# Optimization experiments

Hardware: AMD Instinct MI355X
Metric: run time of the kernel (lower is better)

Reference implementation:

```python
import jax, jax.numpy as jnp
import numpy as np
import math

EMBED_DIM = 1024
NUM_HEADS = 16
HEAD_DIM = EMBED_DIM // NUM_HEADS
B, S = 2, 2048


def setup_inputs() -> dict:
    key = jax.random.key(0)
    ks = jax.random.split(key, 13)
    sc = 1.0 / math.sqrt(EMBED_DIM)
    inp = {
        "query": jax.random.normal(ks[0], (B, S, EMBED_DIM), jnp.float32),
        "key": jax.random.normal(ks[1], (B, S, EMBED_DIM), jnp.float32),
        "value": jax.random.normal(ks[2], (B, S, EMBED_DIM), jnp.float32),
        "input_patch_mask": jax.random.randint(ks[3], (B, S), 0, 2, jnp.int32),
        "Wq": jax.random.normal(ks[4], (EMBED_DIM, EMBED_DIM), jnp.float32) * sc,
        "bq": jnp.zeros((EMBED_DIM,), jnp.float32),
        "Wk": jax.random.normal(ks[5], (EMBED_DIM, EMBED_DIM), jnp.float32) * sc,
        "bk": jnp.zeros((EMBED_DIM,), jnp.float32),
        "Wv": jax.random.normal(ks[6], (EMBED_DIM, EMBED_DIM), jnp.float32) * sc,
        "bv": jnp.zeros((EMBED_DIM,), jnp.float32),
        "Wo": jax.random.normal(ks[7], (EMBED_DIM, EMBED_DIM), jnp.float32) * sc,
        "bo": jnp.zeros((EMBED_DIM,), jnp.float32),
    }
    return inp


def _masked_softmax(scores, mask):
    # Equivalent to masked_fill(-inf) -> softmax -> nan_to_num(0.0):
    # fully-masked rows produce exactly 0, without generating NaNs.
    neg_inf = jnp.array(-jnp.inf, scores.dtype)
    s = jnp.where(mask, scores, neg_inf)
    m = jnp.max(s, axis=-1, keepdims=True)
    m_safe = jnp.where(jnp.isfinite(m), m, jnp.zeros_like(m))
    e = jnp.where(mask, jnp.exp(s - m_safe), 0.0)
    denom = jnp.sum(e, axis=-1, keepdims=True)
    denom = jnp.where(denom == 0.0, 1.0, denom)
    return e / denom


def reference(query, key, value, input_patch_mask, Wq, bq, Wk, bk, Wv, bv, Wo, bo):
    b, s, d = query.shape
    h, hd = NUM_HEADS, HEAD_DIM
    q = (query @ Wq.T + bq).reshape(b, s, h, hd).transpose(0, 2, 1, 3)  # [b,h,s,hd]
    k = (key @ Wk.T + bk).reshape(b, s, h, hd).transpose(0, 2, 1, 3)
    v = (value @ Wv.T + bv).reshape(b, s, h, hd).transpose(0, 2, 1, 3)
    scores = jnp.einsum("bhqd,bhkd->bhqk", q, k) / math.sqrt(hd)
    # mask[b,i,j] = patch_mask[b,i] * patch_mask[b,j]
    mask = (input_patch_mask[:, :, None] * input_patch_mask[:, None, :]) > 0
    attn = _masked_softmax(scores, mask[:, None, :, :])  # dropout in eval mode = identity
    context = jnp.einsum("bhqk,bhkd->bhqd", attn, v)
    context = context.transpose(0, 2, 1, 3).reshape(b, s, d)
    return context @ Wo.T + bo
```

## Files before the change

kernel.cpp:

```cpp
#include <hip/hip_runtime.h>
#include <cstdint>
#include <cstddef>

#define EMBED 1024
#define NHEAD 16
#define HD    64
#define BATCH 2
#define SEQ   2048
#define MROWS (BATCH*SEQ)
#define QSCALE 0.1803368801111137f

typedef __bf16 bf16;
typedef __bf16 bf16x8 __attribute__((ext_vector_type(8)));
typedef float  f32x4  __attribute__((ext_vector_type(4)));
typedef unsigned int u32;

#if __has_builtin(__builtin_amdgcn_exp2f)
#define EXP2(x) __builtin_amdgcn_exp2f(x)
#else
#define EXP2(x) exp2f(x)
#endif

typedef const u32 __attribute__((address_space(1)))* gp_t;
typedef u32 __attribute__((address_space(3)))* lp_t;

__device__ __forceinline__ void g2l16(const void* g, void* l) {
  __builtin_amdgcn_global_load_lds((gp_t)(uintptr_t)g, (lp_t)(u32)(uintptr_t)l, 16, 0, 0);
}

#define MFMA(a, b, c) __builtin_amdgcn_mfma_f32_16x16x32_bf16((a), (b), (c), 0, 0, 0)

#define SZX8 ((MROWS*EMBED)/8)
#define SZW8 ((EMBED*EMBED)/8)

__global__ void cast_all(const float* __restrict__ q, const float* __restrict__ k,
                         const float* __restrict__ v, const float* __restrict__ wq,
                         const float* __restrict__ wk, const float* __restrict__ wv,
                         const float* __restrict__ wo,
                         bf16* xq, bf16* xk, bf16* xv,
                         bf16* wqb, bf16* wkb, bf16* wvb, bf16* wob) {
  int z = blockIdx.y;
  const float* in; bf16* out;
  switch (z) {
    case 0: in = q;  out = xq;  break;
    case 1: in = k;  out = xk;  break;
    case 2: in = v;  out = xv;  break;
    case 3: in = wq; out = wqb; break;
    case 4: in = wk; out = wkb; break;
    case 5: in = wv; out = wvb; break;
    default: in = wo; out = wob; break;
  }
  int n8 = (z < 3) ? SZX8 : SZW8;
  int i = blockIdx.x * blockDim.x + threadIdx.x;
  if (i >= n8) return;
  const float4* p = (const float4*)in;
  float4 a = p[2*i], b = p[2*i+1];
  union { bf16 h[8]; uint4 u; } r;
  r.h[0] = (bf16)a.x; r.h[1] = (bf16)a.y; r.h[2] = (bf16)a.z; r.h[3] = (bf16)a.w;
  r.h[4] = (bf16)b.x; r.h[5] = (bf16)b.y; r.h[6] = (bf16)b.z; r.h[7] = (bf16)b.w;
  ((uint4*)out)[i] = r.u;
}

#define BM 128
#define BN 128
#define BK 32
#define NKI (EMBED/BK)

__device__ __forceinline__ void gemm_core(
    const bf16* __restrict__ A, const bf16* __restrict__ W,
    bf16* Al, bf16* Bl, f32x4 (&acc)[4][4])
{
  const int tid  = threadIdx.x;
  const int lane = tid & 63, wid = tid >> 6;
  const int quad = lane >> 4, l16 = lane & 15;
  const int wm = wid >> 1, wn = wid & 1;
  const int m0 = blockIdx.y * BM, n0 = blockIdx.x * BN;

  const int R = tid >> 2, Cc = tid & 3;
  const int gcol = (Cc ^ ((R >> 1) & 3)) * 8;
  const bf16* Ag = A + (size_t)(m0 + R) * EMBED + gcol;
  const bf16* Bg = W + (size_t)(n0 + R) * EMBED + gcol;
  bf16* AlW = Al + wid * 512;
  bf16* BlW = Bl + wid * 512;

  g2l16(Ag, AlW);                      g2l16(Ag + (size_t)64*EMBED, AlW + 2048);
  g2l16(Bg, BlW);                      g2l16(Bg + (size_t)64*EMBED, BlW + 2048);
  __syncthreads();

  for (int ki = 0; ki < NKI; ++ki) {
    const int cur = ki & 1;
    if (ki + 1 < NKI) {
      const int nb = cur ^ 1;
      const int k0 = (ki + 1) * BK;
      g2l16(Ag + k0, AlW + nb*4096);
      g2l16(Ag + (size_t)64*EMBED + k0, AlW + nb*4096 + 2048);
      g2l16(Bg + k0, BlW + nb*4096);
      g2l16(Bg + (size_t)64*EMBED + k0, BlW + nb*4096 + 2048);
    }
    const bf16* Ac = Al + cur*4096;
    const bf16* Bc = Bl + cur*4096;
    bf16x8 af[4], bg[4];
#pragma unroll
    for (int i = 0; i < 4; ++i) {
      int ra = wm*64 + i*16 + l16;
      af[i] = *(const bf16x8*)(Ac + ra*32 + ((quad ^ ((ra>>1)&3))*8));
      int rb = wn*64 + i*16 + l16;
      bg[i] = *(const bf16x8*)(Bc + rb*32 + ((quad ^ ((rb>>1)&3))*8));
    }
#pragma unroll
    for (int i = 0; i < 4; ++i)
#pragma unroll
      for (int j = 0; j < 4; ++j)
        acc[i][j] = MFMA(af[i], bg[j], acc[i][j]);
    __syncthreads();
  }
}

__global__ __launch_bounds__(256) void qkv_kernel(
    const bf16* __restrict__ Xq, const bf16* __restrict__ Xk, const bf16* __restrict__ Xv,
    const bf16* __restrict__ Wq, const bf16* __restrict__ Wk, const bf16* __restrict__ Wv,
    const float* __restrict__ bq, const float* __restrict__ bk, const float* __restrict__ bv,
    bf16* __restrict__ Qp, bf16* __restrict__ Kp, bf16* __restrict__ VTg)
{
  __shared__ bf16 Al[2*BM*BK];
  __shared__ bf16 Bl[2*BN*BK];
  const int z = blockIdx.z;
  const bf16* A = z==0 ? Xq : z==1 ? Xk : Xv;
  const bf16* W = z==0 ? Wq : z==1 ? Wk : Wv;
  const float* bias = z==0 ? bq : z==1 ? bk : bv;
  const float scale = (z==0) ? QSCALE : 1.0f;

  f32x4 acc[4][4] = {};
  gemm_core(A, W, Al, Bl, acc);

  const int lane = threadIdx.x & 63, wid = threadIdx.x >> 6;
  const int quad = lane >> 4, l16 = lane & 15;
  const int wm = wid >> 1, wn = wid & 1;
  const int m0 = blockIdx.y * BM, n0 = blockIdx.x * BN;

#pragma unroll
  for (int i = 0; i < 4; ++i) {
#pragma unroll
    for (int j = 0; j < 4; ++j) {
      int col = n0 + wn*64 + j*16 + l16;
      float bv2 = bias[col];
      if (z < 2) {
        bf16* outp = (z == 0) ? Qp : Kp;
#pragma unroll
        for (int r = 0; r < 4; ++r) {
          int row = m0 + wm*64 + i*16 + quad*4 + r;
          outp[(size_t)row*EMBED + col] = (bf16)((acc[i][j][r] + bv2) * scale);
        }
      } else {
        int row0 = m0 + wm*64 + i*16 + quad*4;
        int bb = row0 >> 11, ss0 = row0 & (SEQ-1);
        int hh = col >> 6, dd = col & (HD-1);
        const size_t base = (((size_t)bb*NHEAD + hh)*HD + dd)*SEQ;
#pragma unroll
        for (int r = 0; r < 4; ++r) {
          int s = ss0 + r;
          int tile = s >> 6, loc = s & 63;
          int p = ((loc & 15) << 2) | (loc >> 4);
          VTg[base + tile*64 + p] = (bf16)(acc[i][j][r] + bv2);
        }
      }
    }
  }
}

__global__ __launch_bounds__(256) void oproj_kernel(
    const bf16* __restrict__ Ctx, const bf16* __restrict__ Wo,
    const float* __restrict__ bo, float* __restrict__ out)
{
  __shared__ bf16 Al[2*128*32];
  __shared__ bf16 Bl[2*64*32];
  const int tid  = threadIdx.x;
  const int lane = tid & 63, wid = tid >> 6;
  const int quad = lane >> 4, l16 = lane & 15;
  const int m0 = blockIdx.y * 128, n0 = blockIdx.x * 64;

  const int R = tid >> 2, Cc = tid & 3;
  const int gcol = (Cc ^ ((R >> 1) & 3)) * 8;
  const bf16* Ag = Ctx + (size_t)(m0 + R) * EMBED + gcol;
  const bf16* Bg = Wo  + (size_t)(n0 + R) * EMBED + gcol;
  bf16* AlW = Al + wid * 512;
  bf16* BlW = Bl + wid * 512;

  g2l16(Ag, AlW);  g2l16(Ag + (size_t)64*EMBED, AlW + 2048);
  g2l16(Bg, BlW);
  __syncthreads();

  f32x4 acc[2][4] = {};
  for (int ki = 0; ki < NKI; ++ki) {
    const int cur = ki & 1;
    if (ki + 1 < NKI) {
      const int nb = cur ^ 1;
      const int k0 = (ki + 1) * BK;
      g2l16(Ag + k0, AlW + nb*4096);
      g2l16(Ag + (size_t)64*EMBED + k0, AlW + nb*4096 + 2048);
      g2l16(Bg + k0, BlW + nb*2048);
    }
    const bf16* Ac = Al + cur*4096;
    const bf16* Bc = Bl + cur*2048;
    bf16x8 af[2], bg[4];
#pragma unroll
    for (int u = 0; u < 2; ++u) {
      int ra = wid*32 + u*16 + l16;
      af[u] = *(const bf16x8*)(Ac + ra*32 + ((quad ^ ((ra>>1)&3))*8));
    }
#pragma unroll
    for (int j = 0; j < 4; ++j) {
      int rb = j*16 + l16;
      bg[j] = *(const bf16x8*)(Bc + rb*32 + ((quad ^ ((rb>>1)&3))*8));
    }
#pragma unroll
    for (int u = 0; u < 2; ++u)
#pragma unroll
      for (int j = 0; j < 4; ++j)
        acc[u][j] = MFMA(af[u], bg[j], acc[u][j]);
    __syncthreads();
  }

#pragma unroll
  for (int u = 0; u < 2; ++u)
#pragma unroll
    for (int j = 0; j < 4; ++j) {
      int col = n0 + j*16 + l16;
      float bv = bo[col];
#pragma unroll
      for (int r = 0; r < 4; ++r) {
        int row = m0 + wid*32 + u*16 + quad*4 + r;
        out[(size_t)row*EMBED + col] = (acc[u][j][r] + bv);
      }
    }
}

#define NT  (SEQ/64)
#define PST 72

__global__ __launch_bounds__(256, 3) void attn_kernel(
    const bf16* __restrict__ Qp, const bf16* __restrict__ Kp, const bf16* __restrict__ VT,
    const int* __restrict__ pmask, bf16* __restrict__ Ctx)
{
  __shared__ bf16 Kt[2][64*64];
  __shared__ bf16 Vt[2][64*64];
  __shared__ bf16 Pl[4][32*PST];

  const int qt = blockIdx.x, h = blockIdx.y, b = blockIdx.z;
  const int tid = threadIdx.x, lane = tid & 63, wid = tid >> 6;
  const int quad = lane >> 4, l16 = lane & 15;
  const int qrow0 = qt*128 + wid*32;

  bf16x8 qf[2][2];
#pragma unroll
  for (int u = 0; u < 2; ++u) {
    const size_t qoff = (size_t)(b*SEQ + qrow0 + u*16 + l16)*EMBED + h*HD;
    qf[u][0] = *(const bf16x8*)(Qp + qoff + quad*8);
    qf[u][1] = *(const bf16x8*)(Qp + qoff + 32 + quad*8);
  }

  int qm[2][4];
#pragma unroll
  for (int u = 0; u < 2; ++u)
#pragma unroll
    for (int r = 0; r < 4; ++r) qm[u][r] = pmask[b*SEQ + qrow0 + u*16 + quad*4 + r];

  bf16 onev = (bf16)1.0f;
  bf16x8 ones = {onev, onev, onev, onev, onev, onev, onev, onev};

  const bf16* Kg  = Kp + (size_t)b*SEQ*EMBED + h*HD;
  const bf16* VTg = VT + (size_t)(b*NHEAD + h)*HD*SEQ;

  const int R = tid >> 3;
  const int Cc = tid & 7;
  const int scol = (Cc ^ (R & 7)) * 8;

  f32x4 o[2][4] = {};
  f32x4 lacc[2] = {};

#define STAGE(kt, buf) do {                                              \
    const bf16* kg = Kg + (size_t)((kt)*64 + R)*EMBED + scol;            \
    const bf16* vg = VTg + (size_t)R*SEQ + (kt)*64 + scol;               \
    bf16* kl = &Kt[buf][0] + wid*512;                                    \
    bf16* vl = &Vt[buf][0] + wid*512;                                    \
    g2l16(kg, kl);  g2l16(kg + (size_t)32*EMBED, kl + 2048);             \
    g2l16(vg, vl);  g2l16(vg + (size_t)32*SEQ,   vl + 2048);             \
  } while (0)

  STAGE(0, 0);
  __syncthreads();

  for (int kt = 0; kt < NT; ++kt) {
    const int cur = kt & 1;
    if (kt + 1 < NT) STAGE(kt + 1, cur ^ 1);
    const bf16* Kc = &Kt[cur][0];
    const bf16* Vc = &Vt[cur][0];

    f32x4 sg[2][4];
#pragma unroll
    for (int g = 0; g < 4; ++g) {
      int ra = g*16 + l16, sa = ra & 7;
      bf16x8 kfa = *(const bf16x8*)(Kc + ra*64 + ((quad     ^ sa)*8));
      bf16x8 kfb = *(const bf16x8*)(Kc + ra*64 + (((quad+4) ^ sa)*8));
      int km = pmask[b*SEQ + kt*64 + g*16 + l16];
#pragma unroll
      for (int u = 0; u < 2; ++u) {
        f32x4 s = {};
        s = MFMA(qf[u][0], kfa, s);
        s = MFMA(qf[u][1], kfb, s);
#pragma unroll
        for (int r = 0; r < 4; ++r) sg[u][g][r] = km ? EXP2(s[r]) : 0.0f;
      }
    }

#pragma unroll
    for (int u = 0; u < 2; ++u)
#pragma unroll
      for (int r = 0; r < 4; ++r) {
        union { bf16 h[4]; uint2 uu; } pk;
#pragma unroll
        for (int g = 0; g < 4; ++g) pk.h[g] = (bf16)sg[u][g][r];
        *(uint2*)(&Pl[wid][(u*16 + quad*4 + r)*PST + l16*4]) = pk.uu;
      }

    bf16x8 pf[2][2];
#pragma unroll
    for (int u = 0; u < 2; ++u) {
      pf[u][0] = *(const bf16x8*)(&Pl[wid][(u*16 + l16)*PST + quad*8]);
      pf[u][1] = *(const bf16x8*)(&Pl[wid][(u*16 + l16)*PST + 32 + quad*8]);
      lacc[u] = MFMA(pf[u][0], ones, lacc[u]);
      lacc[u] = MFMA(pf[u][1], ones, lacc[u]);
    }
#pragma unroll
    for (int t = 0; t < 4; ++t) {
      int rd = t*16 + l16, sd = rd & 7;
      bf16x8 vf0 = *(const bf16x8*)(Vc + rd*64 + ((quad     ^ sd)*8));
      bf16x8 vf1 = *(const bf16x8*)(Vc + rd*64 + (((quad+4) ^ sd)*8));
#pragma unroll
      for (int u = 0; u < 2; ++u) {
        o[u][t] = MFMA(pf[u][0], vf0, o[u][t]);
        o[u][t] = MFMA(pf[u][1], vf1, o[u][t]);
      }
    }
    __syncthreads();
  }

#pragma unroll
  for (int u = 0; u < 2; ++u) {
    float inv[4];
#pragma unroll
    for (int r = 0; r < 4; ++r)
      inv[r] = (qm[u][r] && lacc[u][r] > 0.f) ? 1.0f / lacc[u][r] : 0.0f;
#pragma unroll
    for (int t = 0; t < 4; ++t)
#pragma unroll
      for (int r = 0; r < 4; ++r) {
        int row = b*SEQ + qrow0 + u*16 + quad*4 + r;
        Ctx[(size_t)row*EMBED + h*HD + t*16 + l16] = (bf16)(o[u][t][r] * inv[r]);
      }
  }
}

extern "C" void kernel_launch(void* const* d_in, const int* in_sizes, int n_in,
                              void* d_out, int out_size, void* d_ws, size_t ws_size,
                              hipStream_t stream)
{
  const float* query = (const float*)d_in[0];
  const float* key   = (const float*)d_in[1];
  const float* value = (const float*)d_in[2];
  const int*   pm    = (const int*)d_in[3];
  const float* Wq = (const float*)d_in[4];
  const float* bq = (const float*)d_in[5];
  const float* Wk = (const float*)d_in[6];
  const float* bk = (const float*)d_in[7];
  const float* Wv = (const float*)d_in[8];
  const float* bv = (const float*)d_in[9];
  const float* Wo = (const float*)d_in[10];
  const float* bo = (const float*)d_in[11];
  float* out = (float*)d_out;

  const size_t SZ_X = (size_t)MROWS * EMBED;
  const size_t SZ_W = (size_t)EMBED * EMBED;

  bf16* p   = (bf16*)d_ws;
  bf16* Xq  = p; p += SZ_X;
  bf16* Xk  = p; p += SZ_X;
  bf16* Xv  = p; p += SZ_X;
  bf16* Wqb = p; p += SZ_W;
  bf16* Wkb = p; p += SZ_W;
  bf16* Wvb = p; p += SZ_W;
  bf16* Wob = p; p += SZ_W;
  bf16* Qp  = p; p += SZ_X;
  bf16* Kp  = p; p += SZ_X;
  bf16* VTg = p; p += SZ_X;
  bf16* Ctx = p; p += SZ_X;

  dim3 gc((unsigned)(SZX8/256), 7);
  cast_all<<<gc, 256, 0, stream>>>(query, key, value, Wq, Wk, Wv, Wo,
                                   Xq, Xk, Xv, Wqb, Wkb, Wvb, Wob);

  dim3 gq(EMBED/BN, MROWS/BM, 3);
  qkv_kernel<<<gq, 256, 0, stream>>>(Xq, Xk, Xv, Wqb, Wkb, Wvb, bq, bk, bv, Qp, Kp, VTg);

  dim3 ga(SEQ/128, NHEAD, BATCH);
  attn_kernel<<<ga, 256, 0, stream>>>(Qp, Kp, VTg, pm, Ctx);

  dim3 gg(EMBED/64, MROWS/128);
  oproj_kernel<<<gg, 256, 0, stream>>>(Ctx, Wob, bo, out);
}
```

Before: 234.7 us.

## Split attention block across 8 waves with 16 query rows each

The attention kernel now launches 512 threads per block, and each of 8 waves handles 16 query rows instead of 4 waves handling 32. K/V staging is spread over twice as many threads, so each thread issues one load per tensor instead of two. The intent is more waves in flight to hide LDS and MFMA latency, with lower register pressure per thread. The trade-off is that each K/V tile loaded into LDS is reused by fewer MFMAs per wave, and the block carries more synchronization overhead.

```diff
diff --git a/kernel.cpp b/kernel.cpp
--- a/kernel.cpp
+++ b/kernel.cpp
@@ -238,32 +238,26 @@
 #define NT  (SEQ/64)
 #define PST 72
 
-__global__ __launch_bounds__(256, 3) void attn_kernel(
+__global__ __launch_bounds__(512, 4) void attn_kernel(
     const bf16* __restrict__ Qp, const bf16* __restrict__ Kp, const bf16* __restrict__ VT,
     const int* __restrict__ pmask, bf16* __restrict__ Ctx)
 {
   __shared__ bf16 Kt[2][64*64];
   __shared__ bf16 Vt[2][64*64];
-  __shared__ bf16 Pl[4][32*PST];
+  __shared__ bf16 Pl[8][16*PST];
 
   const int qt = blockIdx.x, h = blockIdx.y, b = blockIdx.z;
   const int tid = threadIdx.x, lane = tid & 63, wid = tid >> 6;
   const int quad = lane >> 4, l16 = lane & 15;
-  const int qrow0 = qt*128 + wid*32;
-
-  bf16x8 qf[2][2];
-#pragma unroll
-  for (int u = 0; u < 2; ++u) {
-    const size_t qoff = (size_t)(b*SEQ + qrow0 + u*16 + l16)*EMBED + h*HD;
-    qf[u][0] = *(const bf16x8*)(Qp + qoff + quad*8);
-    qf[u][1] = *(const bf16x8*)(Qp + qoff + 32 + quad*8);
-  }
-
-  int qm[2][4];
-#pragma unroll
-  for (int u = 0; u < 2; ++u)
-#pragma unroll
-    for (int r = 0; r < 4; ++r) qm[u][r] = pmask[b*SEQ + qrow0 + u*16 + quad*4 + r];
+  const int qrow0 = qt*128 + wid*16;
+
+  const size_t qoff = (size_t)(b*SEQ + qrow0 + l16)*EMBED + h*HD;
+  bf16x8 qf0 = *(const bf16x8*)(Qp + qoff + quad*8);
+  bf16x8 qf1 = *(const bf16x8*)(Qp + qoff + 32 + quad*8);
+
+  int qm[4];
+#pragma unroll
+  for (int r = 0; r < 4; ++r) qm[r] = pmask[b*SEQ + qrow0 + quad*4 + r];
 
   bf16 onev = (bf16)1.0f;
   bf16x8 ones = {onev, onev, onev, onev, onev, onev, onev, onev};
@@ -275,16 +269,12 @@
   const int Cc = tid & 7;
   const int scol = (Cc ^ (R & 7)) * 8;
 
-  f32x4 o[2][4] = {};
-  f32x4 lacc[2] = {};
+  f32x4 o[4] = {};
+  f32x4 lacc = {};
 
 #define STAGE(kt, buf) do {                                              \
-    const bf16* kg = Kg + (size_t)((kt)*64 + R)*EMBED + scol;            \
-    const bf16* vg = VTg + (size_t)R*SEQ + (kt)*64 + scol;               \
-    bf16* kl = &Kt[buf][0] + wid*512;                                    \
-    bf16* vl = &Vt[buf][0] + wid*512;                                    \
-    g2l16(kg, kl);  g2l16(kg + (size_t)32*EMBED, kl + 2048);             \
-    g2l16(vg, vl);  g2l16(vg + (size_t)32*SEQ,   vl + 2048);             \
+    g2l16(Kg + (size_t)((kt)*64 + R)*EMBED + scol, &Kt[buf][0] + wid*512); \
+    g2l16(VTg + (size_t)R*SEQ + (kt)*64 + scol,    &Vt[buf][0] + wid*512); \
   } while (0)
 
   STAGE(0, 0);
@@ -296,69 +286,55 @@
     const bf16* Kc = &Kt[cur][0];
     const bf16* Vc = &Vt[cur][0];
 
-    f32x4 sg[2][4];
+    f32x4 sg[4];
 #pragma unroll
     for (int g = 0; g < 4; ++g) {
       int ra = g*16 + l16, sa = ra & 7;
       bf16x8 kfa = *(const bf16x8*)(Kc + ra*64 + ((quad     ^ sa)*8));
       bf16x8 kfb = *(const bf16x8*)(Kc + ra*64 + (((quad+4) ^ sa)*8));
       int km = pmask[b*SEQ + kt*64 + g*16 + l16];
-#pragma unroll
-      for (int u = 0; u < 2; ++u) {
-        f32x4 s = {};
-        s = MFMA(qf[u][0], kfa, s);
-        s = MFMA(qf[u][1], kfb, s);
-#pragma unroll
-        for (int r = 0; r < 4; ++r) sg[u][g][r] = km ? EXP2(s[r]) : 0.0f;
-      }
-    }
-
-#pragma unroll
-    for (int u = 0; u < 2; ++u)
-#pragma unroll
-      for (int r = 0; r < 4; ++r) {
-        union { bf16 h[4]; uint2 uu; } pk;
-#pragma unroll
-        for (int g = 0; g < 4; ++g) pk.h[g] = (bf16)sg[u][g][r];
-        *(uint2*)(&Pl[wid][(u*16 + quad*4 + r)*PST + l16*4]) = pk.uu;
-      }
-
-    bf16x8 pf[2][2];
-#pragma unroll
-    for (int u = 0; u < 2; ++u) {
-      pf[u][0] = *(const bf16x8*)(&Pl[wid][(u*16 + l16)*PST + quad*8]);
-      pf[u][1] = *(const bf16x8*)(&Pl[wid][(u*16 + l16)*PST + 32 + quad*8]);
-      lacc[u] = MFMA(pf[u][0], ones, lacc[u]);
-      lacc[u] = MFMA(pf[u][1], ones, lacc[u]);
-    }
+      f32x4 s = {};
+      s = MFMA(qf0, kfa, s);
+      s = MFMA(qf1, kfb, s);
+#pragma unroll
+      for (int r = 0; r < 4; ++r) sg[g][r] = km ? EXP2(s[r]) : 0.0f;
+    }
+
+#pragma unroll
+    for (int r = 0; r < 4; ++r) {
+      union { bf16 h[4]; uint2 uu; } pk;
+#pragma unroll
+      for (int g = 0; g < 4; ++g) pk.h[g] = (bf16)sg[g][r];
+      *(uint2*)(&Pl[wid][(quad*4 + r)*PST + l16*4]) = pk.uu;
+    }
+
+    bf16x8 pf0 = *(const bf16x8*)(&Pl[wid][l16*PST + quad*8]);
+    bf16x8 pf1 = *(const bf16x8*)(&Pl[wid][l16*PST + 32 + quad*8]);
+    lacc = MFMA(pf0, ones, lacc);
+    lacc = MFMA(pf1, ones, lacc);
 #pragma unroll
     for (int t = 0; t < 4; ++t) {
       int rd = t*16 + l16, sd = rd & 7;
       bf16x8 vf0 = *(const bf16x8*)(Vc + rd*64 + ((quad     ^ sd)*8));
       bf16x8 vf1 = *(const bf16x8*)(Vc + rd*64 + (((quad+4) ^ sd)*8));
-#pragma unroll
-      for (int u = 0; u < 2; ++u) {
-        o[u][t] = MFMA(pf[u][0], vf0, o[u][t]);
-        o[u][t] = MFMA(pf[u][1], vf1, o[u][t]);
-      }
+      o[t] = MFMA(pf0, vf0, o[t]);
+      o[t] = MFMA(pf1, vf1, o[t]);
     }
     __syncthreads();
   }
 
-#pragma unroll
-  for (int u = 0; u < 2; ++u) {
-    float inv[4];
-#pragma unroll
-    for (int r = 0; r < 4; ++r)
-      inv[r] = (qm[u][r] && lacc[u][r] > 0.f) ? 1.0f / lacc[u][r] : 0.0f;
-#pragma unroll
-    for (int t = 0; t < 4; ++t)
-#pragma unroll
-      for (int r = 0; r < 4; ++r) {
-        int row = b*SEQ + qrow0 + u*16 + quad*4 + r;
-        Ctx[(size_t)row*EMBED + h*HD + t*16 + l16] = (bf16)(o[u][t][r] * inv[r]);
-      }
-  }
+  float inv[4];
+#pragma unroll
+  for (int r = 0; r < 4; ++r)
+    inv[r] = (qm[r] && lacc[r] > 0.f) ? 1.0f / lacc[r] : 0.0f;
+
+#pragma unroll
+  for (int t = 0; t < 4; ++t)
+#pragma unroll
+    for (int r = 0; r < 4; ++r) {
+      int row = b*SEQ + qrow0 + quad*4 + r;
+      Ctx[(size_t)row*EMBED + h*HD + t*16 + l16] = (bf16)(o[t][r] * inv[r]);
+    }
 }
 
 extern "C" void kernel_launch(void* const* d_in, const int* in_sizes, int n_in,
@@ -403,7 +379,7 @@
   qkv_kernel<<<gq, 256, 0, stream>>>(Xq, Xk, Xv, Wqb, Wkb, Wvb, bq, bk, bv, Qp, Kp, VTg);
 
   dim3 ga(SEQ/128, NHEAD, BATCH);
-  attn_kernel<<<ga, 256, 0, stream>>>(Qp, Kp, VTg, pm, Ctx);
+  attn_kernel<<<ga, 512, 0, stream>>>(Qp, Kp, VTg, pm, Ctx);
 
   dim3 gg(EMBED/64, MROWS/128);
   oproj_kernel<<<gg, 256, 0, stream>>>(Ctx, Wob, bo, out);
```

Measured after the change: 238.9 us. About the same (+1.8%).

## Software-pipeline attention PV with next QK tile, precompute additive mask bias

Applied to the files above, without the earlier changes.

The attention loop is restructured so the PV product for the previous tile runs after the QK product of the current tile, with P double-buffered in shared memory and V loaded one stage later than K. The per-element key-mask branch is replaced by an additive -1e30 bias precomputed into shared memory before exp2. The V projection is computed as W·X^T with swapped operands, so the transposed V layout is written with different indexing and the bias is indexed by output row. Occupancy hint drops from 3 to 2 blocks because of the extra LDS and registers, trading latency hiding across blocks for overlap within one.

```diff
diff --git a/kernel.cpp b/kernel.cpp
--- a/kernel.cpp
+++ b/kernel.cpp
@@ -68,13 +68,12 @@
 
 __device__ __forceinline__ void gemm_core(
     const bf16* __restrict__ A, const bf16* __restrict__ W,
-    bf16* Al, bf16* Bl, f32x4 (&acc)[4][4])
+    int m0, int n0, bf16* Al, bf16* Bl, f32x4 (&acc)[4][4])
 {
   const int tid  = threadIdx.x;
   const int lane = tid & 63, wid = tid >> 6;
   const int quad = lane >> 4, l16 = lane & 15;
   const int wm = wid >> 1, wn = wid & 1;
-  const int m0 = blockIdx.y * BM, n0 = blockIdx.x * BN;
 
   const int R = tid >> 2, Cc = tid & 3;
   const int gcol = (Cc ^ ((R >> 1) & 3)) * 8;
@@ -125,26 +124,27 @@
   __shared__ bf16 Al[2*BM*BK];
   __shared__ bf16 Bl[2*BN*BK];
   const int z = blockIdx.z;
-  const bf16* A = z==0 ? Xq : z==1 ? Xk : Xv;
-  const bf16* W = z==0 ? Wq : z==1 ? Wk : Wv;
+  const bf16* A = z==0 ? Xq : z==1 ? Xk : Wv;
+  const bf16* W = z==0 ? Wq : z==1 ? Wk : Xv;
   const float* bias = z==0 ? bq : z==1 ? bk : bv;
   const float scale = (z==0) ? QSCALE : 1.0f;
+  const int m0 = (z < 2) ? blockIdx.y * BM : blockIdx.x * BM;
+  const int n0 = (z < 2) ? blockIdx.x * BN : blockIdx.y * BN;
 
   f32x4 acc[4][4] = {};
-  gemm_core(A, W, Al, Bl, acc);
+  gemm_core(A, W, m0, n0, Al, Bl, acc);
 
   const int lane = threadIdx.x & 63, wid = threadIdx.x >> 6;
   const int quad = lane >> 4, l16 = lane & 15;
   const int wm = wid >> 1, wn = wid & 1;
-  const int m0 = blockIdx.y * BM, n0 = blockIdx.x * BN;
 
 #pragma unroll
   for (int i = 0; i < 4; ++i) {
 #pragma unroll
     for (int j = 0; j < 4; ++j) {
       int col = n0 + wn*64 + j*16 + l16;
-      float bv2 = bias[col];
       if (z < 2) {
+        float bv2 = bias[col];
         bf16* outp = (z == 0) ? Qp : Kp;
 #pragma unroll
         for (int r = 0; r < 4; ++r) {
@@ -152,16 +152,16 @@
           outp[(size_t)row*EMBED + col] = (bf16)((acc[i][j][r] + bv2) * scale);
         }
       } else {
-        int row0 = m0 + wm*64 + i*16 + quad*4;
-        int bb = row0 >> 11, ss0 = row0 & (SEQ-1);
-        int hh = col >> 6, dd = col & (HD-1);
-        const size_t base = (((size_t)bb*NHEAD + hh)*HD + dd)*SEQ;
+        int t  = col;
+        int bb = t >> 11, ss = t & (SEQ-1);
+        int tile = ss >> 6;
+        int ppos = l16*4 + (j & 3);
 #pragma unroll
         for (int r = 0; r < 4; ++r) {
-          int s = ss0 + r;
-          int tile = s >> 6, loc = s & 63;
-          int p = ((loc & 15) << 2) | (loc >> 4);
-          VTg[base + tile*64 + p] = (bf16)(acc[i][j][r] + bv2);
+          int e = m0 + wm*64 + i*16 + quad*4 + r;
+          int hh = e >> 6, dd = e & (HD-1);
+          VTg[(((size_t)bb*NHEAD + hh)*HD + dd)*SEQ + tile*64 + ppos]
+              = (bf16)(acc[i][j][r] + bias[e]);
         }
       }
     }
@@ -238,19 +238,33 @@
 #define NT  (SEQ/64)
 #define PST 72
 
-__global__ __launch_bounds__(256, 3) void attn_kernel(
+__global__ __launch_bounds__(256, 2) void attn_kernel(
     const bf16* __restrict__ Qp, const bf16* __restrict__ Kp, const bf16* __restrict__ VT,
     const int* __restrict__ pmask, bf16* __restrict__ Ctx)
 {
-  __shared__ bf16 Kt[2][64*64];
-  __shared__ bf16 Vt[2][64*64];
-  __shared__ bf16 Pl[4][32*PST];
+  __shared__ __align__(16) bf16 Kt[2][64*64];
+  __shared__ __align__(16) bf16 Vt[2][64*64];
+  __shared__ __align__(16) bf16 Pl[2][4][32*PST];
+  __shared__ float Mb[SEQ];
 
   const int qt = blockIdx.x, h = blockIdx.y, b = blockIdx.z;
   const int tid = threadIdx.x, lane = tid & 63, wid = tid >> 6;
   const int quad = lane >> 4, l16 = lane & 15;
   const int qrow0 = qt*128 + wid*32;
 
+  {
+    int i = tid * 8;
+    const int4* pm4 = (const int4*)(pmask + b*SEQ + i);
+    int4 a = pm4[0], c = pm4[1];
+    float4 f0, f1;
+    f0.x = a.x ? 0.f : -1e30f;  f0.y = a.y ? 0.f : -1e30f;
+    f0.z = a.z ? 0.f : -1e30f;  f0.w = a.w ? 0.f : -1e30f;
+    f1.x = c.x ? 0.f : -1e30f;  f1.y = c.y ? 0.f : -1e30f;
+    f1.z = c.z ? 0.f : -1e30f;  f1.w = c.w ? 0.f : -1e30f;
+    *(float4*)(Mb + i)     = f0;
+    *(float4*)(Mb + i + 4) = f1;
+  }
+
   bf16x8 qf[2][2];
 #pragma unroll
   for (int u = 0; u < 2; ++u) {
@@ -278,56 +292,91 @@
   f32x4 o[2][4] = {};
   f32x4 lacc[2] = {};
 
-#define STAGE(kt, buf) do {                                              \
-    const bf16* kg = Kg + (size_t)((kt)*64 + R)*EMBED + scol;            \
-    const bf16* vg = VTg + (size_t)R*SEQ + (kt)*64 + scol;               \
-    bf16* kl = &Kt[buf][0] + wid*512;                                    \
-    bf16* vl = &Vt[buf][0] + wid*512;                                    \
-    g2l16(kg, kl);  g2l16(kg + (size_t)32*EMBED, kl + 2048);             \
-    g2l16(vg, vl);  g2l16(vg + (size_t)32*SEQ,   vl + 2048);             \
+#define STAGE_K(kt, buf) do {                                                \
+    const bf16* kg = Kg + (size_t)((kt)*64 + R)*EMBED + scol;                \
+    bf16* kl = &Kt[buf][0] + wid*512;                                        \
+    g2l16(kg, kl);  g2l16(kg + (size_t)32*EMBED, kl + 2048);                 \
   } while (0)
-
-  STAGE(0, 0);
+#define STAGE_V(kt, buf) do {                                                \
+    const bf16* vg = VTg + (size_t)R*SEQ + (kt)*64 + scol;                   \
+    bf16* vl = &Vt[buf][0] + wid*512;                                        \
+    g2l16(vg, vl);  g2l16(vg + (size_t)32*SEQ, vl + 2048);                   \
+  } while (0)
+
+  STAGE_K(0, 0);
   __syncthreads();
 
+#pragma unroll 2
   for (int kt = 0; kt < NT; ++kt) {
     const int cur = kt & 1;
-    if (kt + 1 < NT) STAGE(kt + 1, cur ^ 1);
+    if (kt + 1 < NT) STAGE_K(kt + 1, cur ^ 1);
+    STAGE_V(kt, cur);
+
     const bf16* Kc = &Kt[cur][0];
-    const bf16* Vc = &Vt[cur][0];
-
     f32x4 sg[2][4];
 #pragma unroll
     for (int g = 0; g < 4; ++g) {
       int ra = g*16 + l16, sa = ra & 7;
       bf16x8 kfa = *(const bf16x8*)(Kc + ra*64 + ((quad     ^ sa)*8));
       bf16x8 kfb = *(const bf16x8*)(Kc + ra*64 + (((quad+4) ^ sa)*8));
-      int km = pmask[b*SEQ + kt*64 + g*16 + l16];
 #pragma unroll
       for (int u = 0; u < 2; ++u) {
         f32x4 s = {};
         s = MFMA(qf[u][0], kfa, s);
         s = MFMA(qf[u][1], kfb, s);
-#pragma unroll
-        for (int r = 0; r < 4; ++r) sg[u][g][r] = km ? EXP2(s[r]) : 0.0f;
-      }
-    }
-
-#pragma unroll
-    for (int u = 0; u < 2; ++u)
+        sg[u][g] = s;
+      }
+    }
+
+    if (kt > 0) {
+      const bf16* Vc = &Vt[cur ^ 1][0];
+      bf16x8 pf[2][2];
+#pragma unroll
+      for (int u = 0; u < 2; ++u) {
+        const bf16* Pw = &Pl[cur ^ 1][wid][u*16*PST];
+        pf[u][0] = *(const bf16x8*)(Pw + l16*PST + quad*8);
+        pf[u][1] = *(const bf16x8*)(Pw + l16*PST + 32 + quad*8);
+        lacc[u] = MFMA(pf[u][0], ones, lacc[u]);
+        lacc[u] = MFMA(pf[u][1], ones, lacc[u]);
+      }
+#pragma unroll
+      for (int t = 0; t < 4; ++t) {
+        int rd = t*16 + l16, sd = rd & 7;
+        bf16x8 vf0 = *(const bf16x8*)(Vc + rd*64 + ((quad     ^ sd)*8));
+        bf16x8 vf1 = *(const bf16x8*)(Vc + rd*64 + (((quad+4) ^ sd)*8));
+#pragma unroll
+        for (int u = 0; u < 2; ++u) {
+          o[u][t] = MFMA(pf[u][0], vf0, o[u][t]);
+          o[u][t] = MFMA(pf[u][1], vf1, o[u][t]);
+        }
+      }
+    }
+
+    float bias[4];
+#pragma unroll
+    for (int g = 0; g < 4; ++g) bias[g] = Mb[kt*64 + g*16 + l16];
+#pragma unroll
+    for (int u = 0; u < 2; ++u) {
+      bf16* Pw = &Pl[cur][wid][u*16*PST];
 #pragma unroll
       for (int r = 0; r < 4; ++r) {
         union { bf16 h[4]; uint2 uu; } pk;
 #pragma unroll
-        for (int g = 0; g < 4; ++g) pk.h[g] = (bf16)sg[u][g][r];
-        *(uint2*)(&Pl[wid][(u*16 + quad*4 + r)*PST + l16*4]) = pk.uu;
-      }
-
+        for (int g = 0; g < 4; ++g) pk.h[g] = (bf16)EXP2(sg[u][g][r] + bias[g]);
+        *(uint2*)(Pw + (quad*4 + r)*PST + l16*4) = pk.uu;
+      }
+    }
+    __syncthreads();
+  }
+
+  {
+    const bf16* Vc = &Vt[(NT - 1) & 1][0];
     bf16x8 pf[2][2];
 #pragma unroll
     for (int u = 0; u < 2; ++u) {
-      pf[u][0] = *(const bf16x8*)(&Pl[wid][(u*16 + l16)*PST + quad*8]);
-      pf[u][1] = *(const bf16x8*)(&Pl[wid][(u*16 + l16)*PST + 32 + quad*8]);
+      const bf16* Pw = &Pl[(NT - 1) & 1][wid][u*16*PST];
+      pf[u][0] = *(const bf16x8*)(Pw + l16*PST + quad*8);
+      pf[u][1] = *(const bf16x8*)(Pw + l16*PST + 32 + quad*8);
       lacc[u] = MFMA(pf[u][0], ones, lacc[u]);
       lacc[u] = MFMA(pf[u][1], ones, lacc[u]);
     }
@@ -342,7 +391,6 @@
         o[u][t] = MFMA(pf[u][1], vf1, o[u][t]);
       }
     }
-    __syncthreads();
   }
 
 #pragma unroll
```

New measurement: 225.9 us. 3.7% less time.
